# Kernel optimization log

Measured on AMD Instinct MI355X. Metric: run time of the kernel, lower is better.

The kernel has to match this reference:

```python
import jax, jax.numpy as jnp
import numpy as np

N_NODES = 100000
N_EDGES = 1600000
N_GRAPHS = 2048
D = 128
H = 128
EPS = 1e-5


def gcn_conv(x, src, dst, W, b, n):
    # x: [N, Din], W: [Din, Dout]; GCN with added self-loops and symmetric norm
    xw = x @ W                                       # [N, Dout]
    deg = jnp.zeros((n,), x.dtype).at[dst].add(1.0) + 1.0  # deg of A+I (counted on dst)
    dinv = jax.lax.rsqrt(deg)                        # [N]
    norm = dinv[src] * dinv[dst]                     # [E]
    msg = xw[src] * norm[:, None]                    # [E, Dout] gather + scale
    agg = jax.ops.segment_sum(msg, dst, num_segments=n)
    agg = agg + xw * (dinv * dinv)[:, None]          # self-loop contribution
    return agg + b


def gru_step_h0(x, W_ih, W_hh, b_ih, b_hh):
    # single GRU step with h0 = 0 (PyTorch gate order r, z, n)
    h0 = jnp.zeros_like(x)
    gi = x @ W_ih.T + b_ih                           # [G, 3H]
    gh = h0 @ W_hh.T + b_hh                          # [G, 3H] (zeros + b_hh)
    ir, iz, inn = jnp.split(gi, 3, axis=-1)
    hr, hz, hn = jnp.split(gh, 3, axis=-1)
    r = jax.nn.sigmoid(ir + hr)
    z = jax.nn.sigmoid(iz + hz)
    n = jnp.tanh(inn + r * hn)
    return (1.0 - z) * n + z * h0


def setup_inputs() -> dict:
    key = jax.random.key(0)
    ks = jax.random.split(key, 10)
    x = jax.random.normal(ks[0], (N_NODES, D), jnp.float32)
    edge_index = jax.random.randint(ks[1], (2, N_EDGES), 0, N_NODES, jnp.int32)
    batch = jnp.sort(jax.random.randint(ks[2], (N_NODES,), 0, N_GRAPHS, jnp.int32))
    s = 1.0 / np.sqrt(H)
    return {
        "x": x,
        "edge_index": edge_index,
        "batch": batch,
        "W1": jax.random.normal(ks[3], (D, H), jnp.float32) * s,
        "b1": jnp.zeros((H,), jnp.float32),
        "W2": jax.random.normal(ks[4], (H, H), jnp.float32) * s,
        "b2": jnp.zeros((H,), jnp.float32),
        "W_ih": jax.random.normal(ks[5], (3 * H, H), jnp.float32) * s,
        "W_hh": jax.random.normal(ks[6], (3 * H, H), jnp.float32) * s,
        "b_ih": jnp.zeros((3 * H,), jnp.float32),
        "b_hh": jnp.zeros((3 * H,), jnp.float32),
        "W_lin": jax.random.normal(ks[7], (1, H), jnp.float32) * s,
        "b_lin": jnp.zeros((1,), jnp.float32),
    }


def reference(x, edge_index, batch, W1, b1, W2, b2, W_ih, W_hh, b_ih, b_hh, W_lin, b_lin):
    src, dst = edge_index[0], edge_index[1]
    n = x.shape[0]
    h = jax.nn.relu(gcn_conv(x, src, dst, W1, b1, n))
    h = gcn_conv(h, src, dst, W2, b2, n)
    # global_mean_pool over graph ids
    sums = jax.ops.segment_sum(h, batch, num_segments=N_GRAPHS)
    cnts = jax.ops.segment_sum(jnp.ones((n,), h.dtype), batch, num_segments=N_GRAPHS)
    g = sums / jnp.maximum(cnts, 1.0)[:, None]       # [G, H]
    # dropout p=0.5 in eval mode -> identity
    g = gru_step_h0(g, W_ih, W_hh, b_ih, b_hh)
    g = jax.nn.relu(g)
    mu = jnp.mean(g, axis=-1, keepdims=True)
    var = jnp.mean(jnp.square(g - mu), axis=-1, keepdims=True)
    g = (g - mu) * jax.lax.rsqrt(var + EPS)          # layer_norm, no affine
    return g @ W_lin.T + b_lin                       # [G, 1]
```

## Files before the change

kernel.cpp:

```cpp
#include <hip/hip_runtime.h>
#include <hip/hip_bf16.h>
#include <math.h>

#define DHID 128
#define SH 7
#define BIN_T 2048
#define CAPSH 12
#define SRC_SH 13

typedef __attribute__((ext_vector_type(8))) short bf16x8;
typedef __attribute__((ext_vector_type(4))) float f32x4;

__device__ __forceinline__ int atomAddI(int* p, int v) {
    return __hip_atomic_fetch_add(p, v, __ATOMIC_RELAXED, __HIP_MEMORY_SCOPE_AGENT);
}
__device__ __forceinline__ float bf_lo(unsigned u) { return __uint_as_float(u << 16); }
__device__ __forceinline__ float bf_hi(unsigned u) { return __uint_as_float(u & 0xffff0000u); }
__device__ __forceinline__ float bf_us(unsigned short u) { return __uint_as_float((unsigned)u << 16); }
__device__ __forceinline__ unsigned short bf16_1(float f) {
    unsigned u = __float_as_uint(f);
    u += 0x7fffu + ((u >> 16) & 1u);
    return (unsigned short)(u >> 16);
}
__device__ __forceinline__ unsigned pack_bf16x2(float a, float b) {
    unsigned ua = __float_as_uint(a);
    unsigned ub = __float_as_uint(b);
    ua = (ua + 0x7fffu + ((ua >> 16) & 1u)) >> 16;
    ub = (ub + 0x7fffu + ((ub >> 16) & 1u)) & 0xffff0000u;
    return ua | ub;
}

__global__ __launch_bounds__(256) void bin_edges(const int* __restrict__ src,
                                                 const int* __restrict__ dst,
                                                 int* __restrict__ bcur,
                                                 unsigned* __restrict__ staged,
                                                 const float* __restrict__ W1,
                                                 const float* __restrict__ W2,
                                                 const float* __restrict__ Wih,
                                                 unsigned short* __restrict__ Wt1,
                                                 unsigned short* __restrict__ Wt2,
                                                 unsigned short* __restrict__ Wihb,
                                                 int E, int NB, int nb_bin) {
    int t = threadIdx.x;
    if (blockIdx.x >= nb_bin) {
        int idx = (blockIdx.x - nb_bin) * 256 + t;
        if (idx < 16384) {
            int k = idx >> 7, n = idx & 127;
            Wt1[n * 128 + k] = bf16_1(W1[idx]);
        } else if (idx < 32768) {
            int j = idx - 16384;
            int k = j >> 7, n = j & 127;
            Wt2[n * 128 + k] = bf16_1(W2[j]);
        } else if (idx < 32768 + 49152) {
            int j = idx - 32768;
            Wihb[j] = bf16_1(Wih[j]);
        }
        return;
    }
    __shared__ int lh[1024], lbase[1024], lcur[1024];
    int e0 = blockIdx.x * BIN_T;
    int eend = min(e0 + BIN_T, E);
    for (int i = t; i < NB; i += 256) { lh[i] = 0; lcur[i] = 0; }
    __syncthreads();
    int sv[8], dv[8];
#pragma unroll
    for (int i = 0; i < 8; i++) {
        int e = e0 + t + i * 256;
        if (e < eend) { sv[i] = src[e]; dv[i] = dst[e]; }
        else { sv[i] = 0; dv[i] = -1; }
    }
#pragma unroll
    for (int i = 0; i < 8; i++)
        if (dv[i] >= 0) atomicAdd(&lh[dv[i] >> SH], 1);
    __syncthreads();
    for (int i = t; i < NB; i += 256)
        lbase[i] = lh[i] ? atomAddI(&bcur[i], lh[i]) : 0;
    __syncthreads();
#pragma unroll
    for (int i = 0; i < 8; i++) {
        if (dv[i] >= 0) {
            int d = dv[i];
            int b = d >> SH;
            int pos = lbase[b] + atomicAdd(&lcur[b], 1);
            staged[((size_t)b << CAPSH) + pos] =
                (unsigned)sv[i] | ((unsigned)(d & ((1 << SH) - 1)) << 24);
        }
    }
}

__global__ __launch_bounds__(256) void scatter_gemm(const unsigned* __restrict__ staged,
                                                    const int* __restrict__ bcur,
                                                    int* __restrict__ off,
                                                    float* __restrict__ dinv,
                                                    int* __restrict__ rec,
                                                    int N, int E, int NB,
                                                    const float* __restrict__ Xf,
                                                    const unsigned short* __restrict__ Wt,
                                                    unsigned short* __restrict__ Y) {
    __shared__ __align__(16) unsigned char smem[52224];
    const int tid = threadIdx.x;
    if (blockIdx.x < NB) {
        int* hist = (int*)smem;
        int* sh   = (int*)(smem + 8192);
        int t = tid;
        int b = blockIdx.x;
        int node0 = b << SH;

        int s0 = (t < b) ? bcur[t] : 0;
        int s1 = (256 + t < b) ? bcur[256 + t] : 0;
        int s2 = (512 + t < b) ? bcur[512 + t] : 0;
        int s3 = (768 + t < b) ? bcur[768 + t] : 0;
        int s = s0 + s1 + s2 + s3;
#pragma unroll
        for (int o = 1; o < 64; o <<= 1) s += __shfl_xor(s, o);
        if ((t & 63) == 0) sh[t >> 6] = s;
        __syncthreads();
        int base = sh[0] + sh[1] + sh[2] + sh[3];
        __syncthreads();

        for (int i = t; i < 2048; i += 256) hist[i] = 0;
        __syncthreads();
        int cnt_b = bcur[b];
        const unsigned* st = staged + ((size_t)b << CAPSH);
        for (int j = t; j < cnt_b; j += 256) {
            unsigned w = st[j];
            int key = (int)((w >> 24) << 4) | (int)((w & 0xFFFFFFu) >> SRC_SH);
            atomicAdd(&hist[key], 1);
        }
        __syncthreads();

        int loc[16];
        int run = 0;
        if (t < 128) {
            int base16 = t * 16;
#pragma unroll
            for (int i = 0; i < 16; i++) { loc[i] = run; run += hist[base16 + i]; }
        }
        sh[t] = (t < 128) ? run : 0;
        __syncthreads();
#pragma unroll
        for (int o = 1; o < 256; o <<= 1) {
            int x = (t >= o) ? sh[t - o] : 0;
            __syncthreads();
            sh[t] += x;
            __syncthreads();
        }
        int excl = sh[t] - run;
        if (t < 128) {
            int base16 = t * 16;
#pragma unroll
            for (int i = 0; i < 16; i++) hist[base16 + i] = base + excl + loc[i];
            int node = node0 + t;
            if (node < N) {
                off[node] = base + excl;
                dinv[node] = rsqrtf((float)run + 1.0f);
            }
        }
        if (b == NB - 1 && t == 0) off[N] = E;
        __syncthreads();

        for (int j = t; j < cnt_b; j += 256) {
            unsigned w = st[j];
            int key = (int)((w >> 24) << 4) | (int)((w & 0xFFFFFFu) >> SRC_SH);
            int pos = atomicAdd(&hist[key], 1);
            rec[pos] = (int)(w & 0xFFFFFFu);
        }
    } else {
        unsigned short* Xs = (unsigned short*)smem;
        unsigned short* Ws = (unsigned short*)(smem + 17408);
        {
            const uint4* W4 = (const uint4*)Wt;
#pragma unroll
            for (int i = 0; i < 8; i++) {
                int idx = tid + i * 256;
                int r = idx >> 4, c8 = idx & 15;
                *(uint4*)&Ws[r * 136 + c8 * 8] = W4[idx];
            }
        }
        const int row0 = (blockIdx.x - NB) * 64;
        {
            const float4* X4 = (const float4*)Xf;
#pragma unroll
            for (int i = 0; i < 8; i++) {
                int idx = tid + i * 256;
                int r = idx >> 5, c4 = idx & 31;
                float4 v = make_float4(0.f, 0.f, 0.f, 0.f);
                if (row0 + r < N) v = X4[(size_t)(row0 + r) * 32 + c4];
                uint2 pk = make_uint2(pack_bf16x2(v.x, v.y), pack_bf16x2(v.z, v.w));
                *(uint2*)&Xs[r * 136 + c4 * 4] = pk;
            }
        }
        __syncthreads();

        const int lane = tid & 63;
        const int wv = tid >> 6;
        const int m = lane & 15, quad = lane >> 4;
        const int wrow = wv * 16;

        f32x4 acc[8];
#pragma unroll
        for (int i = 0; i < 8; i++) acc[i] = (f32x4){0.f, 0.f, 0.f, 0.f};

#pragma unroll
        for (int kc = 0; kc < 4; kc++) {
            bf16x8 a = *(const bf16x8*)&Xs[(wrow + m) * 136 + kc * 32 + quad * 8];
#pragma unroll
            for (int nt = 0; nt < 8; nt++) {
                bf16x8 bfr = *(const bf16x8*)&Ws[(nt * 16 + m) * 136 + kc * 32 + quad * 8];
                acc[nt] = __builtin_amdgcn_mfma_f32_16x16x32_bf16(a, bfr, acc[nt], 0, 0, 0);
            }
        }

#pragma unroll
        for (int r = 0; r < 4; r++) {
            int lrow = wrow + quad * 4 + r;
#pragma unroll
            for (int nt = 0; nt < 8; nt++)
                Xs[lrow * 136 + nt * 16 + m] = bf16_1(acc[nt][r]);
        }
        __syncthreads();
#pragma unroll
        for (int i = 0; i < 4; i++) {
            int idx = tid + i * 256;
            int r = idx >> 4, c8 = idx & 15;
            if (row0 + r < N)
                *(uint4*)&Y[(size_t)(row0 + r) * DHID + c8 * 8] =
                    *(const uint4*)&Xs[r * 136 + c8 * 8];
        }
    }
}

__global__ __launch_bounds__(256) void aggregate(const unsigned short* __restrict__ A,
                                                 const float* __restrict__ dinv,
                                                 const int* __restrict__ off,
                                                 const int* __restrict__ rec,
                                                 const float* __restrict__ bias,
                                                 unsigned short* __restrict__ Bout,
                                                 int N, int mode) {
    int node = blockIdx.x * 4 + (threadIdx.x >> 6);
    if (node >= N) return;
    int lane = threadIdx.x & 63;
    int q  = lane >> 4;
    int ql = lane & 15;
    float di = dinv[node];
    float2 acc[4];
    if (q == 0) {
        float s = di * di;
        uint4 v = ((const uint4*)(A + (size_t)node * DHID))[ql];
        const float4* bb = (const float4*)(bias + ql * 8);
        float4 b0 = bb[0], b1 = bb[1];
        acc[0] = make_float2(bf_lo(v.x) * s + b0.x, bf_hi(v.x) * s + b0.y);
        acc[1] = make_float2(bf_lo(v.y) * s + b0.z, bf_hi(v.y) * s + b0.w);
        acc[2] = make_float2(bf_lo(v.z) * s + b1.x, bf_hi(v.z) * s + b1.y);
        acc[3] = make_float2(bf_lo(v.w) * s + b1.z, bf_hi(v.w) * s + b1.w);
    } else {
#pragma unroll
        for (int i = 0; i < 4; i++) acc[i] = make_float2(0.f, 0.f);
    }
    int j = off[node] + q;
    int jend = off[node + 1];
    if (j + 4 < jend) {
        int s0 = rec[j], s1 = rec[j + 4];
        for (; j + 12 < jend; j += 8) {
            int n0 = rec[j + 8], n1 = rec[j + 12];
            uint4 v0 = ((const uint4*)(A + (size_t)s0 * DHID))[ql];
            uint4 v1 = ((const uint4*)(A + (size_t)s1 * DHID))[ql];
            float w0 = dinv[s0] * di;
            float w1 = dinv[s1] * di;
            acc[0].x += bf_lo(v0.x) * w0 + bf_lo(v1.x) * w1;
            acc[0].y += bf_hi(v0.x) * w0 + bf_hi(v1.x) * w1;
            acc[1].x += bf_lo(v0.y) * w0 + bf_lo(v1.y) * w1;
            acc[1].y += bf_hi(v0.y) * w0 + bf_hi(v1.y) * w1;
            acc[2].x += bf_lo(v0.z) * w0 + bf_lo(v1.z) * w1;
            acc[2].y += bf_hi(v0.z) * w0 + bf_hi(v1.z) * w1;
            acc[3].x += bf_lo(v0.w) * w0 + bf_lo(v1.w) * w1;
            acc[3].y += bf_hi(v0.w) * w0 + bf_hi(v1.w) * w1;
            s0 = n0; s1 = n1;
        }
        {
            uint4 v0 = ((const uint4*)(A + (size_t)s0 * DHID))[ql];
            uint4 v1 = ((const uint4*)(A + (size_t)s1 * DHID))[ql];
            float w0 = dinv[s0] * di;
            float w1 = dinv[s1] * di;
            acc[0].x += bf_lo(v0.x) * w0 + bf_lo(v1.x) * w1;
            acc[0].y += bf_hi(v0.x) * w0 + bf_hi(v1.x) * w1;
            acc[1].x += bf_lo(v0.y) * w0 + bf_lo(v1.y) * w1;
            acc[1].y += bf_hi(v0.y) * w0 + bf_hi(v1.y) * w1;
            acc[2].x += bf_lo(v0.z) * w0 + bf_lo(v1.z) * w1;
            acc[2].y += bf_hi(v0.z) * w0 + bf_hi(v1.z) * w1;
            acc[3].x += bf_lo(v0.w) * w0 + bf_lo(v1.w) * w1;
            acc[3].y += bf_hi(v0.w) * w0 + bf_hi(v1.w) * w1;
            j += 8;
        }
    }
    if (j < jend) {
        int s0 = rec[j];
        uint4 v0 = ((const uint4*)(A + (size_t)s0 * DHID))[ql];
        float w0 = dinv[s0] * di;
        acc[0].x += bf_lo(v0.x) * w0;
        acc[0].y += bf_hi(v0.x) * w0;
        acc[1].x += bf_lo(v0.y) * w0;
        acc[1].y += bf_hi(v0.y) * w0;
        acc[2].x += bf_lo(v0.z) * w0;
        acc[2].y += bf_hi(v0.z) * w0;
        acc[3].x += bf_lo(v0.w) * w0;
        acc[3].y += bf_hi(v0.w) * w0;
    }
#pragma unroll
    for (int i = 0; i < 4; i++) {
        acc[i].x += __shfl_xor(acc[i].x, 16);
        acc[i].y += __shfl_xor(acc[i].y, 16);
        acc[i].x += __shfl_xor(acc[i].x, 32);
        acc[i].y += __shfl_xor(acc[i].y, 32);
    }
    if (q == 0) {
        if (mode == 1) {
#pragma unroll
            for (int i = 0; i < 4; i++) {
                acc[i].x = fmaxf(acc[i].x, 0.f);
                acc[i].y = fmaxf(acc[i].y, 0.f);
            }
        }
        uint4 pk;
        pk.x = pack_bf16x2(acc[0].x, acc[0].y);
        pk.y = pack_bf16x2(acc[1].x, acc[1].y);
        pk.z = pack_bf16x2(acc[2].x, acc[2].y);
        pk.w = pack_bf16x2(acc[3].x, acc[3].y);
        ((uint4*)(Bout + (size_t)node * DHID))[ql] = pk;
    }
}

__global__ __launch_bounds__(256) void gemm_mfma(const void* __restrict__ Xv,
                                                 const unsigned short* __restrict__ Wt,
                                                 unsigned short* __restrict__ Y,
                                                 int N, int x_is_bf16,
                                                 int wstride, int ystride) {
    __shared__ unsigned short Xs[64 * 136];
    __shared__ unsigned short Ws[128 * 136];
    const int tid = threadIdx.x;
    const unsigned short* Wg = Wt + (size_t)blockIdx.y * wstride;
    unsigned short* Yg = Y + (size_t)blockIdx.y * ystride;

    {
        const uint4* W4 = (const uint4*)Wg;
#pragma unroll
        for (int i = 0; i < 8; i++) {
            int idx = tid + i * 256;
            int r = idx >> 4, c8 = idx & 15;
            *(uint4*)&Ws[r * 136 + c8 * 8] = W4[idx];
        }
    }
    const int row0 = blockIdx.x * 64;
    if (x_is_bf16) {
        const uint4* X4 = (const uint4*)Xv;
#pragma unroll
        for (int i = 0; i < 4; i++) {
            int idx = tid + i * 256;
            int r = idx >> 4, c8 = idx & 15;
            uint4 v = make_uint4(0u, 0u, 0u, 0u);
            if (row0 + r < N) v = X4[(size_t)(row0 + r) * 16 + c8];
            *(uint4*)&Xs[r * 136 + c8 * 8] = v;
        }
    } else {
        const float4* X4 = (const float4*)Xv;
#pragma unroll
        for (int i = 0; i < 8; i++) {
            int idx = tid + i * 256;
            int r = idx >> 5, c4 = idx & 31;
            float4 v = make_float4(0.f, 0.f, 0.f, 0.f);
            if (row0 + r < N) v = X4[(size_t)(row0 + r) * 32 + c4];
            uint2 pk = make_uint2(pack_bf16x2(v.x, v.y), pack_bf16x2(v.z, v.w));
            *(uint2*)&Xs[r * 136 + c4 * 4] = pk;
        }
    }
    __syncthreads();

    const int lane = tid & 63;
    const int wv = tid >> 6;
    const int m = lane & 15, quad = lane >> 4;
    const int wrow = wv * 16;

    f32x4 acc[8];
#pragma unroll
    for (int i = 0; i < 8; i++) acc[i] = (f32x4){0.f, 0.f, 0.f, 0.f};

#pragma unroll
    for (int kc = 0; kc < 4; kc++) {
        bf16x8 a = *(const bf16x8*)&Xs[(wrow + m) * 136 + kc * 32 + quad * 8];
#pragma unroll
        for (int nt = 0; nt < 8; nt++) {
            bf16x8 b = *(const bf16x8*)&Ws[(nt * 16 + m) * 136 + kc * 32 + quad * 8];
            acc[nt] = __builtin_amdgcn_mfma_f32_16x16x32_bf16(a, b, acc[nt], 0, 0, 0);
        }
    }

#pragma unroll
    for (int r = 0; r < 4; r++) {
        int lrow = wrow + quad * 4 + r;
#pragma unroll
        for (int nt = 0; nt < 8; nt++)
            Xs[lrow * 136 + nt * 16 + m] = bf16_1(acc[nt][r]);
    }
    __syncthreads();
#pragma unroll
    for (int i = 0; i < 4; i++) {
        int idx = tid + i * 256;
        int r = idx >> 4, c8 = idx & 15;
        if (row0 + r < N)
            *(uint4*)&Yg[(size_t)(row0 + r) * DHID + c8 * 8] =
                *(const uint4*)&Xs[r * 136 + c8 * 8];
    }
}

__global__ __launch_bounds__(256) void tail_head(const unsigned short* __restrict__ B,
                                                 const int* __restrict__ batch,
                                                 const unsigned short* __restrict__ Wihb,
                                                 const float* __restrict__ b_ih,
                                                 const float* __restrict__ b_hh,
                                                 const float* __restrict__ W_lin,
                                                 const float* __restrict__ b_lin,
                                                 float* __restrict__ out,
                                                 int N, int G) {
    __shared__ float grow[128];
    __shared__ float psum[4][128];
    __shared__ float gi[384];
    __shared__ float red[4];
    __shared__ int se[2];
    const int t = threadIdx.x;
    const int g = blockIdx.x;
    if (t < 2) {
        int target = g + t, lo = 0, hi = N;
        while (lo < hi) {
            int mid = (lo + hi) >> 1;
            if (batch[mid] < target) lo = mid + 1; else hi = mid;
        }
        se[t] = lo;
    }
    __syncthreads();
    const int s = se[0], e = se[1];

    const int c2 = t & 63;
    const int rh = t >> 6;
    float sx = 0.f, sy = 0.f;
    for (int r = s + rh; r < e; r += 4) {
        unsigned u = *(const unsigned*)(B + (size_t)r * DHID + c2 * 2);
        sx += bf_lo(u);
        sy += bf_hi(u);
    }
    *(float2*)&psum[rh][c2 * 2] = make_float2(sx, sy);
    __syncthreads();
    if (t < 128) {
        grow[t] = (psum[0][t] + psum[1][t] + psum[2][t] + psum[3][t]) /
                  fmaxf((float)(e - s), 1.0f);
    }
    __syncthreads();

    {
        float a0 = 0.f;
        const uint4* wr = (const uint4*)(Wihb + (size_t)t * DHID);
#pragma unroll
        for (int k8 = 0; k8 < 16; k8++) {
            uint4 wv = wr[k8];
            const float* gk = &grow[k8 * 8];
            a0 += bf_lo(wv.x) * gk[0] + bf_hi(wv.x) * gk[1]
                + bf_lo(wv.y) * gk[2] + bf_hi(wv.y) * gk[3]
                + bf_lo(wv.z) * gk[4] + bf_hi(wv.z) * gk[5]
                + bf_lo(wv.w) * gk[6] + bf_hi(wv.w) * gk[7];
        }
        gi[t] = a0;
    }
    if (t < 128) {
        float a1 = 0.f;
        const uint4* wr = (const uint4*)(Wihb + (size_t)(256 + t) * DHID);
#pragma unroll
        for (int k8 = 0; k8 < 16; k8++) {
            uint4 wv = wr[k8];
            const float* gk = &grow[k8 * 8];
            a1 += bf_lo(wv.x) * gk[0] + bf_hi(wv.x) * gk[1]
                + bf_lo(wv.y) * gk[2] + bf_hi(wv.y) * gk[3]
                + bf_lo(wv.z) * gk[4] + bf_hi(wv.z) * gk[5]
                + bf_lo(wv.w) * gk[6] + bf_hi(wv.w) * gk[7];
        }
        gi[256 + t] = a1;
    }
    __syncthreads();

    float y = 0.f, wl = 0.f;
    if (t < 128) {
        float d0 = gi[t], d1 = gi[128 + t], d2 = gi[256 + t];
        float rg = 1.f / (1.f + expf(-(d0 + b_ih[t] + b_hh[t])));
        float zg = 1.f / (1.f + expf(-(d1 + b_ih[128 + t] + b_hh[128 + t])));
        float ng = tanhf(d2 + b_ih[256 + t] + rg * b_hh[256 + t]);
        y = fmaxf((1.f - zg) * ng, 0.f);
        wl = W_lin[t];
    }
    auto blockSum = [&](float v) -> float {
#pragma unroll
        for (int o = 1; o < 64; o <<= 1) v += __shfl_xor(v, o);
        __syncthreads();
        if ((t & 63) == 0) red[t >> 6] = v;
        __syncthreads();
        return red[0] + red[1] + red[2] + red[3];
    };
    float mu = blockSum(y) * (1.f / 128.f);
    float dy = (t < 128) ? (y - mu) : 0.f;
    float var = blockSum(dy * dy) * (1.f / 128.f);
    float yn = dy * rsqrtf(var + 1e-5f);
    float tot = blockSum(yn * wl);
    if (t == 0) out[g] = tot + b_lin[0];
}

extern "C" void kernel_launch(void* const* d_in, const int* in_sizes, int n_in,
                              void* d_out, int out_size, void* d_ws, size_t ws_size,
                              hipStream_t stream) {
    const float* x     = (const float*)d_in[0];
    const int*   ei    = (const int*)d_in[1];
    const int*   batch = (const int*)d_in[2];
    const float* W1    = (const float*)d_in[3];
    const float* b1    = (const float*)d_in[4];
    const float* W2    = (const float*)d_in[5];
    const float* b2    = (const float*)d_in[6];
    const float* W_ih  = (const float*)d_in[7];
    const float* b_ih  = (const float*)d_in[9];
    const float* b_hh  = (const float*)d_in[10];
    const float* W_lin = (const float*)d_in[11];
    const float* b_lin = (const float*)d_in[12];
    float* out = (float*)d_out;

    const int N = in_sizes[0] / DHID;
    const int E = in_sizes[1] / 2;
    const int G = out_size;
    const int* src = ei;
    const int* dst = ei + E;
    const int NB = (N + (1 << SH) - 1) >> SH;

    auto align256 = [](size_t v) { return (v + 255) & ~(size_t)255; };
    char* p = (char*)d_ws;
    size_t used = 0;
    auto carve = [&](size_t bytes) -> char* {
        char* q = p + used;
        used += align256(bytes);
        return q;
    };

    int*   off    = (int*)carve(((size_t)N + 1) * 4);
    int*   bcur   = (int*)carve(1024 * 4);
    float* dinv   = (float*)carve((size_t)N * 4);
    unsigned* staged = (unsigned*)carve(((size_t)NB << CAPSH) * 4);
    int*   rec    = (int*)carve((size_t)E * 4);
    unsigned short* Wt1  = (unsigned short*)carve((size_t)128 * 128 * 2);
    unsigned short* Wt2  = (unsigned short*)carve((size_t)128 * 128 * 2);
    unsigned short* Wihb = (unsigned short*)carve((size_t)3 * 128 * 128 * 2);
    unsigned short* A    = (unsigned short*)carve((size_t)N * DHID * 2);
    unsigned short* B1b  = (unsigned short*)carve((size_t)N * DHID * 2);
    size_t matB = (size_t)N * DHID * 2;
    unsigned short* B2b;
    if (ws_size >= used + matB) {
        B2b = (unsigned short*)carve(matB);
    } else {
        B2b = (unsigned short*)d_in[0];
    }

    dim3 blk(256);
    int nb_g  = (N + 63) / 64;
    int nb_ag = (N + 3) / 4;
    int nb_bin = (E + BIN_T - 1) / BIN_T;
    int nb_wp  = (81920 + 255) / 256;

    hipMemsetAsync(bcur, 0, 1024 * 4, stream);
    bin_edges<<<nb_bin + nb_wp, blk, 0, stream>>>(src, dst, bcur, staged,
                                                  W1, W2, W_ih, Wt1, Wt2, Wihb,
                                                  E, NB, nb_bin);
    scatter_gemm<<<NB + nb_g, blk, 0, stream>>>(staged, bcur, off, dinv, rec,
                                                N, E, NB, x, Wt1, A);

    aggregate<<<nb_ag, blk, 0, stream>>>(A, dinv, off, rec, b1, B1b, N, 1);

    gemm_mfma<<<dim3(nb_g, 1), blk, 0, stream>>>(B1b, Wt2, A, N, 1, 0, 0);
    aggregate<<<nb_ag, blk, 0, stream>>>(A, dinv, off, rec, b2, B2b, N, 0);

    tail_head<<<G, blk, 0, stream>>>(B2b, batch, Wihb, b_ih, b_hh, W_lin, b_lin,
                                     out, N, G);
}
```

Before: 339.8 us.

## Reassociate layer-2 GEMM after mean pooling and fuse aggregation with pooling

Uses linearity to move the second GCN weight multiply after the graph mean pool. The node-level GEMM is dropped and replaced by a small per-graph matvec in the tail kernel. The second aggregation now pools directly into a per-graph fp32 buffer with atomics, pre-scaled by inverse counts computed in the binning kernel. This removes a full N×128 GEMM and the write and read of the B2 intermediate, at the cost of atomic contention on the pooled buffer and a different rounding order.

```diff
diff --git a/kernel.cpp b/kernel.cpp
--- a/kernel.cpp
+++ b/kernel.cpp
@@ -16,7 +16,6 @@
 }
 __device__ __forceinline__ float bf_lo(unsigned u) { return __uint_as_float(u << 16); }
 __device__ __forceinline__ float bf_hi(unsigned u) { return __uint_as_float(u & 0xffff0000u); }
-__device__ __forceinline__ float bf_us(unsigned short u) { return __uint_as_float((unsigned)u << 16); }
 __device__ __forceinline__ unsigned short bf16_1(float f) {
     unsigned u = __float_as_uint(f);
     u += 0x7fffu + ((u >> 16) & 1u);
@@ -40,7 +39,9 @@
                                                  unsigned short* __restrict__ Wt1,
                                                  unsigned short* __restrict__ Wt2,
                                                  unsigned short* __restrict__ Wihb,
-                                                 int E, int NB, int nb_bin) {
+                                                 const int* __restrict__ batch,
+                                                 float* __restrict__ cnt_inv,
+                                                 int E, int NB, int nb_bin, int Nn, int G) {
     int t = threadIdx.x;
     if (blockIdx.x >= nb_bin) {
         int idx = (blockIdx.x - nb_bin) * 256 + t;
@@ -54,6 +55,14 @@
         } else if (idx < 32768 + 49152) {
             int j = idx - 32768;
             Wihb[j] = bf16_1(Wih[j]);
+        } else if (idx < 81920 + G) {
+            int g = idx - 81920;
+            int lo = 0, hi = Nn;
+            while (lo < hi) { int mid = (lo + hi) >> 1; if (batch[mid] < g) lo = mid + 1; else hi = mid; }
+            int s = lo;
+            hi = Nn;
+            while (lo < hi) { int mid = (lo + hi) >> 1; if (batch[mid] < g + 1) lo = mid + 1; else hi = mid; }
+            cnt_inv[g] = 1.0f / fmaxf((float)(lo - s), 1.0f);
         }
         return;
     }
@@ -330,128 +339,127 @@
     }
 }
 
-__global__ __launch_bounds__(256) void gemm_mfma(const void* __restrict__ Xv,
-                                                 const unsigned short* __restrict__ Wt,
-                                                 unsigned short* __restrict__ Y,
-                                                 int N, int x_is_bf16,
-                                                 int wstride, int ystride) {
-    __shared__ unsigned short Xs[64 * 136];
-    __shared__ unsigned short Ws[128 * 136];
-    const int tid = threadIdx.x;
-    const unsigned short* Wg = Wt + (size_t)blockIdx.y * wstride;
-    unsigned short* Yg = Y + (size_t)blockIdx.y * ystride;
-
-    {
-        const uint4* W4 = (const uint4*)Wg;
-#pragma unroll
-        for (int i = 0; i < 8; i++) {
-            int idx = tid + i * 256;
-            int r = idx >> 4, c8 = idx & 15;
-            *(uint4*)&Ws[r * 136 + c8 * 8] = W4[idx];
-        }
-    }
-    const int row0 = blockIdx.x * 64;
-    if (x_is_bf16) {
-        const uint4* X4 = (const uint4*)Xv;
-#pragma unroll
-        for (int i = 0; i < 4; i++) {
-            int idx = tid + i * 256;
-            int r = idx >> 4, c8 = idx & 15;
-            uint4 v = make_uint4(0u, 0u, 0u, 0u);
-            if (row0 + r < N) v = X4[(size_t)(row0 + r) * 16 + c8];
-            *(uint4*)&Xs[r * 136 + c8 * 8] = v;
-        }
+__global__ __launch_bounds__(256) void aggregate_pool(const unsigned short* __restrict__ A,
+                                                      const float* __restrict__ dinv,
+                                                      const int* __restrict__ off,
+                                                      const int* __restrict__ rec,
+                                                      const int* __restrict__ batch,
+                                                      const float* __restrict__ cnt_inv,
+                                                      float* __restrict__ gbuf,
+                                                      int N) {
+    int node = blockIdx.x * 4 + (threadIdx.x >> 6);
+    if (node >= N) return;
+    int lane = threadIdx.x & 63;
+    int q  = lane >> 4;
+    int ql = lane & 15;
+    float di = dinv[node];
+    float2 acc[4];
+    if (q == 0) {
+        float s = di * di;
+        uint4 v = ((const uint4*)(A + (size_t)node * DHID))[ql];
+        acc[0] = make_float2(bf_lo(v.x) * s, bf_hi(v.x) * s);
+        acc[1] = make_float2(bf_lo(v.y) * s, bf_hi(v.y) * s);
+        acc[2] = make_float2(bf_lo(v.z) * s, bf_hi(v.z) * s);
+        acc[3] = make_float2(bf_lo(v.w) * s, bf_hi(v.w) * s);
     } else {
-        const float4* X4 = (const float4*)Xv;
-#pragma unroll
-        for (int i = 0; i < 8; i++) {
-            int idx = tid + i * 256;
-            int r = idx >> 5, c4 = idx & 31;
-            float4 v = make_float4(0.f, 0.f, 0.f, 0.f);
-            if (row0 + r < N) v = X4[(size_t)(row0 + r) * 32 + c4];
-            uint2 pk = make_uint2(pack_bf16x2(v.x, v.y), pack_bf16x2(v.z, v.w));
-            *(uint2*)&Xs[r * 136 + c4 * 4] = pk;
-        }
-    }
-    __syncthreads();
-
-    const int lane = tid & 63;
-    const int wv = tid >> 6;
-    const int m = lane & 15, quad = lane >> 4;
-    const int wrow = wv * 16;
-
-    f32x4 acc[8];
-#pragma unroll
-    for (int i = 0; i < 8; i++) acc[i] = (f32x4){0.f, 0.f, 0.f, 0.f};
-
-#pragma unroll
-    for (int kc = 0; kc < 4; kc++) {
-        bf16x8 a = *(const bf16x8*)&Xs[(wrow + m) * 136 + kc * 32 + quad * 8];
-#pragma unroll
-        for (int nt = 0; nt < 8; nt++) {
-            bf16x8 b = *(const bf16x8*)&Ws[(nt * 16 + m) * 136 + kc * 32 + quad * 8];
-            acc[nt] = __builtin_amdgcn_mfma_f32_16x16x32_bf16(a, b, acc[nt], 0, 0, 0);
-        }
-    }
-
-#pragma unroll
-    for (int r = 0; r < 4; r++) {
-        int lrow = wrow + quad * 4 + r;
-#pragma unroll
-        for (int nt = 0; nt < 8; nt++)
-            Xs[lrow * 136 + nt * 16 + m] = bf16_1(acc[nt][r]);
-    }
-    __syncthreads();
+#pragma unroll
+        for (int i = 0; i < 4; i++) acc[i] = make_float2(0.f, 0.f);
+    }
+    int j = off[node] + q;
+    int jend = off[node + 1];
+    if (j + 4 < jend) {
+        int s0 = rec[j], s1 = rec[j + 4];
+        for (; j + 12 < jend; j += 8) {
+            int n0 = rec[j + 8], n1 = rec[j + 12];
+            uint4 v0 = ((const uint4*)(A + (size_t)s0 * DHID))[ql];
+            uint4 v1 = ((const uint4*)(A + (size_t)s1 * DHID))[ql];
+            float w0 = dinv[s0] * di;
+            float w1 = dinv[s1] * di;
+            acc[0].x += bf_lo(v0.x) * w0 + bf_lo(v1.x) * w1;
+            acc[0].y += bf_hi(v0.x) * w0 + bf_hi(v1.x) * w1;
+            acc[1].x += bf_lo(v0.y) * w0 + bf_lo(v1.y) * w1;
+            acc[1].y += bf_hi(v0.y) * w0 + bf_hi(v1.y) * w1;
+            acc[2].x += bf_lo(v0.z) * w0 + bf_lo(v1.z) * w1;
+            acc[2].y += bf_hi(v0.z) * w0 + bf_hi(v1.z) * w1;
+            acc[3].x += bf_lo(v0.w) * w0 + bf_lo(v1.w) * w1;
+            acc[3].y += bf_hi(v0.w) * w0 + bf_hi(v1.w) * w1;
+            s0 = n0; s1 = n1;
+        }
+        {
+            uint4 v0 = ((const uint4*)(A + (size_t)s0 * DHID))[ql];
+            uint4 v1 = ((const uint4*)(A + (size_t)s1 * DHID))[ql];
+            float w0 = dinv[s0] * di;
+            float w1 = dinv[s1] * di;
+            acc[0].x += bf_lo(v0.x) * w0 + bf_lo(v1.x) * w1;
+            acc[0].y += bf_hi(v0.x) * w0 + bf_hi(v1.x) * w1;
+            acc[1].x += bf_lo(v0.y) * w0 + bf_lo(v1.y) * w1;
+            acc[1].y += bf_hi(v0.y) * w0 + bf_hi(v1.y) * w1;
+            acc[2].x += bf_lo(v0.z) * w0 + bf_lo(v1.z) * w1;
+            acc[2].y += bf_hi(v0.z) * w0 + bf_hi(v1.z) * w1;
+            acc[3].x += bf_lo(v0.w) * w0 + bf_lo(v1.w) * w1;
+            acc[3].y += bf_hi(v0.w) * w0 + bf_hi(v1.w) * w1;
+            j += 8;
+        }
+    }
+    if (j < jend) {
+        int s0 = rec[j];
+        uint4 v0 = ((const uint4*)(A + (size_t)s0 * DHID))[ql];
+        float w0 = dinv[s0] * di;
+        acc[0].x += bf_lo(v0.x) * w0;
+        acc[0].y += bf_hi(v0.x) * w0;
+        acc[1].x += bf_lo(v0.y) * w0;
+        acc[1].y += bf_hi(v0.y) * w0;
+        acc[2].x += bf_lo(v0.z) * w0;
+        acc[2].y += bf_hi(v0.z) * w0;
+        acc[3].x += bf_lo(v0.w) * w0;
+        acc[3].y += bf_hi(v0.w) * w0;
+    }
 #pragma unroll
     for (int i = 0; i < 4; i++) {
-        int idx = tid + i * 256;
-        int r = idx >> 4, c8 = idx & 15;
-        if (row0 + r < N)
-            *(uint4*)&Yg[(size_t)(row0 + r) * DHID + c8 * 8] =
-                *(const uint4*)&Xs[r * 136 + c8 * 8];
-    }
-}
-
-__global__ __launch_bounds__(256) void tail_head(const unsigned short* __restrict__ B,
-                                                 const int* __restrict__ batch,
+        acc[i].x += __shfl_xor(acc[i].x, 16);
+        acc[i].y += __shfl_xor(acc[i].y, 16);
+        acc[i].x += __shfl_xor(acc[i].x, 32);
+        acc[i].y += __shfl_xor(acc[i].y, 32);
+    }
+    int g = batch[node];
+    float sc = cnt_inv[g];
+    float* dstp = gbuf + (size_t)g * DHID + ql * 8 + 2 * q;
+    atomicAdd(dstp,     acc[q].x * sc);
+    atomicAdd(dstp + 1, acc[q].y * sc);
+}
+
+__global__ __launch_bounds__(256) void tail_head(const float* __restrict__ gbuf,
+                                                 const unsigned short* __restrict__ Wt2,
+                                                 const float* __restrict__ b2,
                                                  const unsigned short* __restrict__ Wihb,
                                                  const float* __restrict__ b_ih,
                                                  const float* __restrict__ b_hh,
                                                  const float* __restrict__ W_lin,
                                                  const float* __restrict__ b_lin,
-                                                 float* __restrict__ out,
-                                                 int N, int G) {
+                                                 float* __restrict__ out, int G) {
     __shared__ float grow[128];
-    __shared__ float psum[4][128];
+    __shared__ float g2[128];
     __shared__ float gi[384];
     __shared__ float red[4];
-    __shared__ int se[2];
     const int t = threadIdx.x;
     const int g = blockIdx.x;
-    if (t < 2) {
-        int target = g + t, lo = 0, hi = N;
-        while (lo < hi) {
-            int mid = (lo + hi) >> 1;
-            if (batch[mid] < target) lo = mid + 1; else hi = mid;
-        }
-        se[t] = lo;
-    }
+
+    if (t < 128) grow[t] = gbuf[(size_t)g * DHID + t];
     __syncthreads();
-    const int s = se[0], e = se[1];
-
-    const int c2 = t & 63;
-    const int rh = t >> 6;
-    float sx = 0.f, sy = 0.f;
-    for (int r = s + rh; r < e; r += 4) {
-        unsigned u = *(const unsigned*)(B + (size_t)r * DHID + c2 * 2);
-        sx += bf_lo(u);
-        sy += bf_hi(u);
-    }
-    *(float2*)&psum[rh][c2 * 2] = make_float2(sx, sy);
-    __syncthreads();
+
     if (t < 128) {
-        grow[t] = (psum[0][t] + psum[1][t] + psum[2][t] + psum[3][t]) /
-                  fmaxf((float)(e - s), 1.0f);
+        float a = 0.f;
+        const uint4* wr = (const uint4*)(Wt2 + (size_t)t * DHID);
+#pragma unroll
+        for (int k8 = 0; k8 < 16; k8++) {
+            uint4 wv = wr[k8];
+            const float* gk = &grow[k8 * 8];
+            a += bf_lo(wv.x) * gk[0] + bf_hi(wv.x) * gk[1]
+               + bf_lo(wv.y) * gk[2] + bf_hi(wv.y) * gk[3]
+               + bf_lo(wv.z) * gk[4] + bf_hi(wv.z) * gk[5]
+               + bf_lo(wv.w) * gk[6] + bf_hi(wv.w) * gk[7];
+        }
+        g2[t] = a + b2[t];
     }
     __syncthreads();
 
@@ -461,7 +469,7 @@
 #pragma unroll
         for (int k8 = 0; k8 < 16; k8++) {
             uint4 wv = wr[k8];
-            const float* gk = &grow[k8 * 8];
+            const float* gk = &g2[k8 * 8];
             a0 += bf_lo(wv.x) * gk[0] + bf_hi(wv.x) * gk[1]
                 + bf_lo(wv.y) * gk[2] + bf_hi(wv.y) * gk[3]
                 + bf_lo(wv.z) * gk[4] + bf_hi(wv.z) * gk[5]
@@ -475,7 +483,7 @@
 #pragma unroll
         for (int k8 = 0; k8 < 16; k8++) {
             uint4 wv = wr[k8];
-            const float* gk = &grow[k8 * 8];
+            const float* gk = &g2[k8 * 8];
             a1 += bf_lo(wv.x) * gk[0] + bf_hi(wv.x) * gk[1]
                 + bf_lo(wv.y) * gk[2] + bf_hi(wv.y) * gk[3]
                 + bf_lo(wv.z) * gk[4] + bf_hi(wv.z) * gk[5]
@@ -545,7 +553,9 @@
 
     int*   off    = (int*)carve(((size_t)N + 1) * 4);
     int*   bcur   = (int*)carve(1024 * 4);
+    float* gbuf   = (float*)carve((size_t)G * DHID * 4);
     float* dinv   = (float*)carve((size_t)N * 4);
+    float* cnt_inv = (float*)carve((size_t)G * 4);
     unsigned* staged = (unsigned*)carve(((size_t)NB << CAPSH) * 4);
     int*   rec    = (int*)carve((size_t)E * 4);
     unsigned short* Wt1  = (unsigned short*)carve((size_t)128 * 128 * 2);
@@ -553,32 +563,26 @@
     unsigned short* Wihb = (unsigned short*)carve((size_t)3 * 128 * 128 * 2);
     unsigned short* A    = (unsigned short*)carve((size_t)N * DHID * 2);
     unsigned short* B1b  = (unsigned short*)carve((size_t)N * DHID * 2);
-    size_t matB = (size_t)N * DHID * 2;
-    unsigned short* B2b;
-    if (ws_size >= used + matB) {
-        B2b = (unsigned short*)carve(matB);
-    } else {
-        B2b = (unsigned short*)d_in[0];
-    }
 
     dim3 blk(256);
     int nb_g  = (N + 63) / 64;
     int nb_ag = (N + 3) / 4;
     int nb_bin = (E + BIN_T - 1) / BIN_T;
-    int nb_wp  = (81920 + 255) / 256;
-
-    hipMemsetAsync(bcur, 0, 1024 * 4, stream);
+    int nb_wp  = (81920 + G + 255) / 256;
+
+    hipMemsetAsync(bcur, 0, 1024 * 4 + (size_t)G * DHID * 4, stream);
     bin_edges<<<nb_bin + nb_wp, blk, 0, stream>>>(src, dst, bcur, staged,
                                                   W1, W2, W_ih, Wt1, Wt2, Wihb,
-                                                  E, NB, nb_bin);
+                                                  batch, cnt_inv,
+                                                  E, NB, nb_bin, N, G);
     scatter_gemm<<<NB + nb_g, blk, 0, stream>>>(staged, bcur, off, dinv, rec,
                                                 N, E, NB, x, Wt1, A);
 
     aggregate<<<nb_ag, blk, 0, stream>>>(A, dinv, off, rec, b1, B1b, N, 1);
 
-    gemm_mfma<<<dim3(nb_g, 1), blk, 0, stream>>>(B1b, Wt2, A, N, 1, 0, 0);
-    aggregate<<<nb_ag, blk, 0, stream>>>(A, dinv, off, rec, b2, B2b, N, 0);
-
-    tail_head<<<G, blk, 0, stream>>>(B2b, batch, Wihb, b_ih, b_hh, W_lin, b_lin,
-                                     out, N, G);
-}
+    aggregate_pool<<<nb_ag, blk, 0, stream>>>(B1b, dinv, off, rec, batch, cnt_inv,
+                                              gbuf, N);
+
+    tail_head<<<G, blk, 0, stream>>>(gbuf, Wt2, b2, Wihb, b_ih, b_hh, W_lin, b_lin,
+                                     out, G);
+}
```

After: 382.3 us. 1.13x slower.

## Defer second-layer weight multiply until after mean pooling

Applied to the files above, without the earlier changes.

Uses linearity to reorder the second GCN layer as aggregate(h1) then pool, and applies W2 and b2 per graph inside the tail kernel instead of on every node. This drops the full node-level MFMA GEMM launch and one N×128 bf16 write and read. The second aggregation now runs with a zeroed bias buffer, and the tail kernel gains a small 128×128 matvec per graph. Rounding changes because the bf16 intermediates now differ.

```diff
diff --git a/kernel.cpp b/kernel.cpp
--- a/kernel.cpp
+++ b/kernel.cpp
@@ -16,7 +16,6 @@
 }
 __device__ __forceinline__ float bf_lo(unsigned u) { return __uint_as_float(u << 16); }
 __device__ __forceinline__ float bf_hi(unsigned u) { return __uint_as_float(u & 0xffff0000u); }
-__device__ __forceinline__ float bf_us(unsigned short u) { return __uint_as_float((unsigned)u << 16); }
 __device__ __forceinline__ unsigned short bf16_1(float f) {
     unsigned u = __float_as_uint(f);
     u += 0x7fffu + ((u >> 16) & 1u);
@@ -330,90 +329,10 @@
     }
 }
 
-__global__ __launch_bounds__(256) void gemm_mfma(const void* __restrict__ Xv,
-                                                 const unsigned short* __restrict__ Wt,
-                                                 unsigned short* __restrict__ Y,
-                                                 int N, int x_is_bf16,
-                                                 int wstride, int ystride) {
-    __shared__ unsigned short Xs[64 * 136];
-    __shared__ unsigned short Ws[128 * 136];
-    const int tid = threadIdx.x;
-    const unsigned short* Wg = Wt + (size_t)blockIdx.y * wstride;
-    unsigned short* Yg = Y + (size_t)blockIdx.y * ystride;
-
-    {
-        const uint4* W4 = (const uint4*)Wg;
-#pragma unroll
-        for (int i = 0; i < 8; i++) {
-            int idx = tid + i * 256;
-            int r = idx >> 4, c8 = idx & 15;
-            *(uint4*)&Ws[r * 136 + c8 * 8] = W4[idx];
-        }
-    }
-    const int row0 = blockIdx.x * 64;
-    if (x_is_bf16) {
-        const uint4* X4 = (const uint4*)Xv;
-#pragma unroll
-        for (int i = 0; i < 4; i++) {
-            int idx = tid + i * 256;
-            int r = idx >> 4, c8 = idx & 15;
-            uint4 v = make_uint4(0u, 0u, 0u, 0u);
-            if (row0 + r < N) v = X4[(size_t)(row0 + r) * 16 + c8];
-            *(uint4*)&Xs[r * 136 + c8 * 8] = v;
-        }
-    } else {
-        const float4* X4 = (const float4*)Xv;
-#pragma unroll
-        for (int i = 0; i < 8; i++) {
-            int idx = tid + i * 256;
-            int r = idx >> 5, c4 = idx & 31;
-            float4 v = make_float4(0.f, 0.f, 0.f, 0.f);
-            if (row0 + r < N) v = X4[(size_t)(row0 + r) * 32 + c4];
-            uint2 pk = make_uint2(pack_bf16x2(v.x, v.y), pack_bf16x2(v.z, v.w));
-            *(uint2*)&Xs[r * 136 + c4 * 4] = pk;
-        }
-    }
-    __syncthreads();
-
-    const int lane = tid & 63;
-    const int wv = tid >> 6;
-    const int m = lane & 15, quad = lane >> 4;
-    const int wrow = wv * 16;
-
-    f32x4 acc[8];
-#pragma unroll
-    for (int i = 0; i < 8; i++) acc[i] = (f32x4){0.f, 0.f, 0.f, 0.f};
-
-#pragma unroll
-    for (int kc = 0; kc < 4; kc++) {
-        bf16x8 a = *(const bf16x8*)&Xs[(wrow + m) * 136 + kc * 32 + quad * 8];
-#pragma unroll
-        for (int nt = 0; nt < 8; nt++) {
-            bf16x8 b = *(const bf16x8*)&Ws[(nt * 16 + m) * 136 + kc * 32 + quad * 8];
-            acc[nt] = __builtin_amdgcn_mfma_f32_16x16x32_bf16(a, b, acc[nt], 0, 0, 0);
-        }
-    }
-
-#pragma unroll
-    for (int r = 0; r < 4; r++) {
-        int lrow = wrow + quad * 4 + r;
-#pragma unroll
-        for (int nt = 0; nt < 8; nt++)
-            Xs[lrow * 136 + nt * 16 + m] = bf16_1(acc[nt][r]);
-    }
-    __syncthreads();
-#pragma unroll
-    for (int i = 0; i < 4; i++) {
-        int idx = tid + i * 256;
-        int r = idx >> 4, c8 = idx & 15;
-        if (row0 + r < N)
-            *(uint4*)&Yg[(size_t)(row0 + r) * DHID + c8 * 8] =
-                *(const uint4*)&Xs[r * 136 + c8 * 8];
-    }
-}
-
 __global__ __launch_bounds__(256) void tail_head(const unsigned short* __restrict__ B,
                                                  const int* __restrict__ batch,
+                                                 const unsigned short* __restrict__ Wt2,
+                                                 const float* __restrict__ b2,
                                                  const unsigned short* __restrict__ Wihb,
                                                  const float* __restrict__ b_ih,
                                                  const float* __restrict__ b_hh,
@@ -423,6 +342,7 @@
                                                  int N, int G) {
     __shared__ float grow[128];
     __shared__ float psum[4][128];
+    __shared__ float g2[128];
     __shared__ float gi[384];
     __shared__ float red[4];
     __shared__ int se[2];
@@ -455,13 +375,29 @@
     }
     __syncthreads();
 
+    if (t < 128) {
+        float a = 0.f;
+        const uint4* wr = (const uint4*)(Wt2 + (size_t)t * DHID);
+#pragma unroll
+        for (int k8 = 0; k8 < 16; k8++) {
+            uint4 wv = wr[k8];
+            const float* gk = &grow[k8 * 8];
+            a += bf_lo(wv.x) * gk[0] + bf_hi(wv.x) * gk[1]
+               + bf_lo(wv.y) * gk[2] + bf_hi(wv.y) * gk[3]
+               + bf_lo(wv.z) * gk[4] + bf_hi(wv.z) * gk[5]
+               + bf_lo(wv.w) * gk[6] + bf_hi(wv.w) * gk[7];
+        }
+        g2[t] = a + b2[t];
+    }
+    __syncthreads();
+
     {
         float a0 = 0.f;
         const uint4* wr = (const uint4*)(Wihb + (size_t)t * DHID);
 #pragma unroll
         for (int k8 = 0; k8 < 16; k8++) {
             uint4 wv = wr[k8];
-            const float* gk = &grow[k8 * 8];
+            const float* gk = &g2[k8 * 8];
             a0 += bf_lo(wv.x) * gk[0] + bf_hi(wv.x) * gk[1]
                 + bf_lo(wv.y) * gk[2] + bf_hi(wv.y) * gk[3]
                 + bf_lo(wv.z) * gk[4] + bf_hi(wv.z) * gk[5]
@@ -475,7 +411,7 @@
 #pragma unroll
         for (int k8 = 0; k8 < 16; k8++) {
             uint4 wv = wr[k8];
-            const float* gk = &grow[k8 * 8];
+            const float* gk = &g2[k8 * 8];
             a1 += bf_lo(wv.x) * gk[0] + bf_hi(wv.x) * gk[1]
                 + bf_lo(wv.y) * gk[2] + bf_hi(wv.y) * gk[3]
                 + bf_lo(wv.z) * gk[4] + bf_hi(wv.z) * gk[5]
@@ -545,6 +481,7 @@
 
     int*   off    = (int*)carve(((size_t)N + 1) * 4);
     int*   bcur   = (int*)carve(1024 * 4);
+    float* zbias  = (float*)carve(128 * 4);
     float* dinv   = (float*)carve((size_t)N * 4);
     unsigned* staged = (unsigned*)carve(((size_t)NB << CAPSH) * 4);
     int*   rec    = (int*)carve((size_t)E * 4);
@@ -567,7 +504,7 @@
     int nb_bin = (E + BIN_T - 1) / BIN_T;
     int nb_wp  = (81920 + 255) / 256;
 
-    hipMemsetAsync(bcur, 0, 1024 * 4, stream);
+    hipMemsetAsync(bcur, 0, 1024 * 4 + 256 + 128 * 4, stream);
     bin_edges<<<nb_bin + nb_wp, blk, 0, stream>>>(src, dst, bcur, staged,
                                                   W1, W2, W_ih, Wt1, Wt2, Wihb,
                                                   E, NB, nb_bin);
@@ -576,9 +513,8 @@
 
     aggregate<<<nb_ag, blk, 0, stream>>>(A, dinv, off, rec, b1, B1b, N, 1);
 
-    gemm_mfma<<<dim3(nb_g, 1), blk, 0, stream>>>(B1b, Wt2, A, N, 1, 0, 0);
-    aggregate<<<nb_ag, blk, 0, stream>>>(A, dinv, off, rec, b2, B2b, N, 0);
-
-    tail_head<<<G, blk, 0, stream>>>(B2b, batch, Wihb, b_ih, b_hh, W_lin, b_lin,
-                                     out, N, G);
-}
+    aggregate<<<nb_ag, blk, 0, stream>>>(B1b, dinv, off, rec, zbias, B2b, N, 0);
+
+    tail_head<<<G, blk, 0, stream>>>(B2b, batch, Wt2, b2, Wihb, b_ih, b_hh,
+                                     W_lin, b_lin, out, N, G);
+}
```

Measured after the change: 331.7 us. -2.4%, faster.
